# Performance work log

Hardware: AMD Instinct MI355X
Metric: run time of the kernel (lower is better)

Reference implementation:

```python
import jax, jax.numpy as jnp
import numpy as np
import math

V, D, H, L, T, B = 50257, 1024, 16, 8, 1024, 4
HD = D // H
EPS = 1e-5


def setup_inputs() -> dict:
    key = jax.random.key(0)
    ks = jax.random.split(key, 8)
    s = 0.02
    inp = {
        'context': jax.random.randint(ks[0], (B, T), 0, V, dtype=jnp.int32),
        'targets': jax.random.randint(ks[1], (B, T), 0, V, dtype=jnp.int32),
        'wte': jax.random.normal(ks[2], (V, D), jnp.float32) * s,  # tied with lm_head
        'wpe': jax.random.normal(ks[3], (T, D), jnp.float32) * s,
        'ln1_g': jnp.ones((L, D), jnp.float32), 'ln1_b': jnp.zeros((L, D), jnp.float32),
        'w_attn': jax.random.normal(ks[4], (L, 3 * D, D), jnp.float32) * s,
        'w_proj': jax.random.normal(ks[5], (L, D, D), jnp.float32) * s,
        'ln2_g': jnp.ones((L, D), jnp.float32), 'ln2_b': jnp.zeros((L, D), jnp.float32),
        'w_fc': jax.random.normal(ks[6], (L, 4 * D, D), jnp.float32) * s,
        'w_out': jax.random.normal(ks[7], (L, D, 4 * D), jnp.float32) * s,
        'lnf_g': jnp.ones((D,), jnp.float32), 'lnf_b': jnp.zeros((D,), jnp.float32),
    }
    return inp


def layer_norm(x, g, b):
    mu = jnp.mean(x, axis=-1, keepdims=True)
    var = jnp.var(x, axis=-1, keepdims=True)
    return (x - mu) * jax.lax.rsqrt(var + EPS) * g + b


def attention(x, w_attn, w_proj):
    # x: [B,T,D]; w_attn: [3D,D] (torch Linear convention: y = x @ W^T)
    qkv = x @ w_attn.T  # [B,T,3D]
    q, k, v = jnp.split(qkv, 3, axis=-1)
    q = q.reshape(B, T, H, HD).transpose(0, 2, 1, 3)  # [B,H,T,hd]
    k = k.reshape(B, T, H, HD).transpose(0, 2, 1, 3)
    v = v.reshape(B, T, H, HD).transpose(0, 2, 1, 3)
    att = jnp.einsum('bhtd,bhsd->bhts', q, k) * (1.0 / math.sqrt(HD))
    causal = jnp.tril(jnp.ones((T, T), dtype=bool))
    att = jnp.where(causal, att, -jnp.inf)
    att = jax.nn.softmax(att, axis=-1)
    y = jnp.einsum('bhts,bhsd->bhtd', att, v)
    y = y.transpose(0, 2, 1, 3).reshape(B, T, D)
    return y @ w_proj.T


def mlp(x, w_fc, w_out):
    h = jax.nn.gelu(x @ w_fc.T, approximate=False)  # exact GELU = torch nn.GELU()
    return h @ w_out.T


def reference(context, targets, wte, wpe, ln1_g, ln1_b, w_attn, w_proj,
              ln2_g, ln2_b, w_fc, w_out, lnf_g, lnf_b):
    x = wte[context] + wpe[jnp.arange(T)]  # [B,T,D]
    for i in range(L):
        x = x + attention(layer_norm(x, ln1_g[i], ln1_b[i]), w_attn[i], w_proj[i])
        x = x + mlp(layer_norm(x, ln2_g[i], ln2_b[i]), w_fc[i], w_out[i])
    x = layer_norm(x, lnf_g, lnf_b)
    logits = x @ wte.T  # tied lm_head, [B,T,V]
    # cross entropy with ignore_index=-1
    logp = jax.nn.log_softmax(logits, axis=-1)
    tgt = targets.reshape(-1)
    valid = tgt != -1
    safe_tgt = jnp.where(valid, tgt, 0)
    nll = -jnp.take_along_axis(logp.reshape(-1, V), safe_tgt[:, None], axis=-1)[:, 0]
    loss = jnp.sum(jnp.where(valid, nll, 0.0)) / jnp.maximum(jnp.sum(valid), 1)
    return logits, loss
```

## Files before the change

### kernel.cpp

```cpp
#include <hip/hip_runtime.h>
#include <cstdint>

#define V_SIZE 50257
#define V_PAD  50432
#define D_DIM  1024
#define H_NUM  16
#define L_NUM  8
#define T_LEN  1024
#define B_NUM  4
#define HD_DIM 64
#define M_ROWS 4096
#define LN_EPS 1e-5f

typedef __attribute__((ext_vector_type(8))) __bf16 bf16x8;
typedef __attribute__((ext_vector_type(4))) float f32x4;
typedef __attribute__((ext_vector_type(8))) unsigned short u16x8;

__device__ __forceinline__ unsigned short f2bf(float f) {
  unsigned u = __builtin_bit_cast(unsigned, f);
  u += 0x7fffu + ((u >> 16) & 1u);
  return (unsigned short)(u >> 16);
}

__device__ __forceinline__ void gload_lds16(const void* g, void* l) {
  typedef const __attribute__((address_space(1))) unsigned int* gp_t;
  typedef __attribute__((address_space(3))) unsigned int* lp_t;
  __builtin_amdgcn_global_load_lds((gp_t)g, (lp_t)l, 16, 0, 0);
}

#define BARSB() { __builtin_amdgcn_s_barrier(); __builtin_amdgcn_sched_barrier(0); }
#define LGKM0() { asm volatile("s_waitcnt lgkmcnt(0)" ::: "memory"); __builtin_amdgcn_sched_barrier(0); }

__global__ __launch_bounds__(256) void embed_kernel(const int* __restrict__ ctx,
                                                    const float* __restrict__ wte,
                                                    const float* __restrict__ wpe,
                                                    float* __restrict__ x) {
  int i = blockIdx.x * blockDim.x + threadIdx.x;
  if (i >= M_ROWS * D_DIM) return;
  int bt = i / D_DIM, d = i - bt * D_DIM;
  int t = bt & (T_LEN - 1);
  x[i] = wte[(size_t)ctx[bt] * D_DIM + d] + wpe[(size_t)t * D_DIM + d];
}

__global__ __launch_bounds__(256) void conv_layer_kernel(const float* __restrict__ wa,
                                                         const float* __restrict__ wp,
                                                         const float* __restrict__ wf,
                                                         const float* __restrict__ wo,
                                                         unsigned short* __restrict__ oa,
                                                         unsigned short* __restrict__ op,
                                                         unsigned short* __restrict__ of,
                                                         unsigned short* __restrict__ oo) {
  long i = (long)(blockIdx.x * 256 + threadIdx.x) * 8;
  const float* src; unsigned short* dst; long off;
  if (i < 3145728L)      { src = wa; dst = oa; off = i; }
  else if (i < 4194304L) { src = wp; dst = op; off = i - 3145728L; }
  else if (i < 8388608L) { src = wf; dst = of; off = i - 4194304L; }
  else                   { src = wo; dst = oo; off = i - 8388608L; }
  float4 v0 = *(const float4*)(src + off);
  float4 v1 = *(const float4*)(src + off + 4);
  u16x8 o;
  o[0] = f2bf(v0.x); o[1] = f2bf(v0.y); o[2] = f2bf(v0.z); o[3] = f2bf(v0.w);
  o[4] = f2bf(v1.x); o[5] = f2bf(v1.y); o[6] = f2bf(v1.z); o[7] = f2bf(v1.w);
  *(u16x8*)(dst + off) = o;
}

__global__ __launch_bounds__(256) void conv_kernel(const float* __restrict__ in,
                                                   unsigned short* __restrict__ out, long n) {
  long i = (long)(blockIdx.x * 256 + threadIdx.x) * 8;
  if (i >= n) return;
  float4 v0 = *(const float4*)(in + i);
  float4 v1 = *(const float4*)(in + i + 4);
  u16x8 o;
  o[0] = f2bf(v0.x); o[1] = f2bf(v0.y); o[2] = f2bf(v0.z); o[3] = f2bf(v0.w);
  o[4] = f2bf(v1.x); o[5] = f2bf(v1.y); o[6] = f2bf(v1.z); o[7] = f2bf(v1.w);
  *(u16x8*)(out + i) = o;
}

__global__ __launch_bounds__(256) void layernorm_kernel(const float* __restrict__ x,
                                                        const float* __restrict__ g,
                                                        const float* __restrict__ b,
                                                        unsigned short* __restrict__ o) {
  int r = blockIdx.x;
  int tid = threadIdx.x;
  const float* row = x + (size_t)r * D_DIM;
  float4 v = *(const float4*)(row + tid * 4);
  float s  = v.x + v.y + v.z + v.w;
  float s2 = v.x * v.x + v.y * v.y + v.z * v.z + v.w * v.w;
  #pragma unroll
  for (int off = 32; off; off >>= 1) {
    s  += __shfl_xor(s, off);
    s2 += __shfl_xor(s2, off);
  }
  __shared__ float a1[4], a2[4];
  int w = tid >> 6, lane = tid & 63;
  if (lane == 0) { a1[w] = s; a2[w] = s2; }
  __syncthreads();
  s  = a1[0] + a1[1] + a1[2] + a1[3];
  s2 = a2[0] + a2[1] + a2[2] + a2[3];
  float mu  = s * (1.0f / D_DIM);
  float var = s2 * (1.0f / D_DIM) - mu * mu;
  float rs  = rsqrtf(var + LN_EPS);
  int d = tid * 4;
  float4 gv = *(const float4*)(g + d);
  float4 bv = *(const float4*)(b + d);
  ushort4 ov;
  ov.x = f2bf((v.x - mu) * rs * gv.x + bv.x);
  ov.y = f2bf((v.y - mu) * rs * gv.y + bv.y);
  ov.z = f2bf((v.z - mu) * rs * gv.z + bv.z);
  ov.w = f2bf((v.w - mu) * rs * gv.w + bv.w);
  *(ushort4*)(o + (size_t)r * D_DIM + d) = ov;
}

template<int EPI>
__global__ __launch_bounds__(256) void mfma_gemm(const unsigned short* __restrict__ A,
                                                 const unsigned short* __restrict__ W,
                                                 const float* R, void* Cout,
                                                 int K, int ldc, int nreal) {
  __shared__ unsigned short As[128 * 32];
  __shared__ unsigned short Bs[128 * 32];
  const int tid  = threadIdx.x;
  const int wave = tid >> 6, lane = tid & 63;
  const int wr = wave >> 1, wc = wave & 1;
  const long row0 = (long)blockIdx.y * 128;
  const long col0 = (long)blockIdx.x * 128;
  f32x4 acc[4][4] = {};
  const int frow = lane & 15;
  const int fk   = (lane >> 4) * 8;
  const int b0 = wave * 2048 + lane * 16;
  for (int k0 = 0; k0 < K; k0 += 32) {
    #pragma unroll
    for (int c = 0; c < 2; ++c) {
      int b = b0 + c * 1024;
      int r = b >> 6, ke = (b & 63) >> 1;
      gload_lds16(A + (row0 + r) * (long)K + k0 + ke, (char*)As + b);
      gload_lds16(W + (col0 + r) * (long)K + k0 + ke, (char*)Bs + b);
    }
    __syncthreads();
    bf16x8 af[4], bfr[4];
    #pragma unroll
    for (int i = 0; i < 4; ++i)
      af[i] = *(const bf16x8*)(As + (wr * 64 + i * 16 + frow) * 32 + fk);
    #pragma unroll
    for (int j = 0; j < 4; ++j)
      bfr[j] = *(const bf16x8*)(Bs + (wc * 64 + j * 16 + frow) * 32 + fk);
    #pragma unroll
    for (int i = 0; i < 4; ++i)
      #pragma unroll
      for (int j = 0; j < 4; ++j)
        acc[i][j] = __builtin_amdgcn_mfma_f32_16x16x32_bf16(af[i], bfr[j], acc[i][j], 0, 0, 0);
    __syncthreads();
  }
  const int crow = (lane >> 4) * 4;
  const int ccol = lane & 15;
  #pragma unroll
  for (int i = 0; i < 4; ++i) {
    #pragma unroll
    for (int r = 0; r < 4; ++r) {
      long row = row0 + wr * 64 + i * 16 + crow + r;
      #pragma unroll
      for (int j = 0; j < 4; ++j) {
        long col = col0 + wc * 64 + j * 16 + ccol;
        float v = acc[i][j][r];
        if (EPI == 1) {
          ((float*)Cout)[row * (long)ldc + col] = v + R[row * (long)ldc + col];
        } else {
          ((float*)Cout)[row * (long)ldc + col] = v;
        }
      }
    }
  }
}

__device__ __forceinline__ void stage_chunk8(const unsigned short* __restrict__ base,
                                             long rbase, int K, long gk,
                                             char* cb, int tid) {
  #pragma unroll
  for (int j = 0; j < 2; ++j) {
    int db = j * 8192 + tid * 16;
    int lb = db ^ (((db >> 7) & 3) << 4);
    long r = lb >> 6;
    int e = (lb & 63) >> 1;
    gload_lds16(base + (rbase + r) * (long)K + gk + e, cb + db);
  }
}

__device__ __forceinline__ bf16x8 rdfrag(const char* cb, int rr, int lhi) {
  int p = (rr << 6) + (lhi << 4);
  p ^= ((rr >> 1) & 3) << 4;
  return *(const bf16x8*)(cb + p);
}

template<int EPI>
__global__ __launch_bounds__(512, 1) void gemm8p(const unsigned short* __restrict__ A,
                                                 const unsigned short* __restrict__ W,
                                                 void* Cout, int K, int ldc, int nreal,
                                                 int nbx, int xcd) {
  __shared__ char lds[131072];
  const int tid  = threadIdx.x;
  const int lane = tid & 63;
  const int wave = tid >> 6;
  const int wr = wave >> 2, wc = wave & 3;
  const int lhi = lane >> 4, llo = lane & 15;
  int bid = blockIdx.x;
  if (xcd) { int per = (int)gridDim.x >> 3; bid = (bid & 7) * per + (bid >> 3); }
  const int brow = bid % nbx;
  const int bcol = bid / nbx;
  const long row0 = (long)brow * 256;
  const long col0 = (long)bcol * 256;
  char* Ab0 = (char*)lds;
  char* Bb0 = (char*)lds + 65536;
  const int nt = K >> 6;

  stage_chunk8(A, row0, K, 0,  Ab0,         tid);
  stage_chunk8(W, col0, K, 0,  Bb0,         tid);
  stage_chunk8(A, row0, K, 32, Ab0 + 16384, tid);
  stage_chunk8(W, col0, K, 32, Bb0 + 16384, tid);
  if (nt > 1) {
    stage_chunk8(W, col0, K, 64, Bb0 + 32768, tid);
    stage_chunk8(A, row0, K, 64, Ab0 + 32768, tid);
    stage_chunk8(W, col0, K, 96, Bb0 + 49152, tid);
    asm volatile("s_waitcnt vmcnt(10)" ::: "memory");
  } else {
    asm volatile("s_waitcnt vmcnt(0)" ::: "memory");
  }
  BARSB();

  f32x4 acc[8][4] = {};
  bf16x8 bb[4];
  for (int t = 0; t < nt; ++t) {
    char* Ac = Ab0 + (t & 1) * 32768;
    char* Bc = Bb0 + (t & 1) * 32768;
    char* An = Ab0 + ((t + 1) & 1) * 32768;
    bf16x8 aa[4];
    #pragma unroll
    for (int m = 0; m < 4; ++m) aa[m] = rdfrag(Ac, wr * 128 + m * 16 + llo, lhi);
    #pragma unroll
    for (int n = 0; n < 4; ++n) bb[n] = rdfrag(Bc, wc * 64 + n * 16 + llo, lhi);
    if (t + 1 < nt) stage_chunk8(A, row0, K, (long)(t + 1) * 64 + 32, An + 16384, tid);
    BARSB(); LGKM0();
    __builtin_amdgcn_s_setprio(1);
    #pragma unroll
    for (int m = 0; m < 4; ++m)
      #pragma unroll
      for (int n = 0; n < 4; ++n)
        acc[m][n] = __builtin_amdgcn_mfma_f32_16x16x32_bf16(aa[m], bb[n], acc[m][n], 0, 0, 0);
    __builtin_amdgcn_s_setprio(0);
    BARSB();
    #pragma unroll
    for (int m = 0; m < 4; ++m) aa[m] = rdfrag(Ac, wr * 128 + 64 + m * 16 + llo, lhi);
    if (t + 2 < nt) stage_chunk8(W, col0, K, (long)(t + 2) * 64, Bc, tid);
    BARSB(); LGKM0();
    __builtin_amdgcn_s_setprio(1);
    #pragma unroll
    for (int m = 0; m < 4; ++m)
      #pragma unroll
      for (int n = 0; n < 4; ++n)
        acc[m + 4][n] = __builtin_amdgcn_mfma_f32_16x16x32_bf16(aa[m], bb[n], acc[m + 4][n], 0, 0, 0);
    __builtin_amdgcn_s_setprio(0);
    if (t <= nt - 3)      { asm volatile("s_waitcnt vmcnt(10)" ::: "memory"); }
    else if (t == nt - 2) { asm volatile("s_waitcnt vmcnt(8)"  ::: "memory"); }
    else                  { asm volatile("s_waitcnt vmcnt(0)"  ::: "memory"); }
    BARSB();
    #pragma unroll
    for (int m = 0; m < 4; ++m) aa[m] = rdfrag(Ac + 16384, wr * 128 + m * 16 + llo, lhi);
    #pragma unroll
    for (int n = 0; n < 4; ++n) bb[n] = rdfrag(Bc + 16384, wc * 64 + n * 16 + llo, lhi);
    if (t + 2 < nt) stage_chunk8(A, row0, K, (long)(t + 2) * 64, Ac, tid);
    BARSB(); LGKM0();
    __builtin_amdgcn_s_setprio(1);
    #pragma unroll
    for (int m = 0; m < 4; ++m)
      #pragma unroll
      for (int n = 0; n < 4; ++n)
        acc[m][n] = __builtin_amdgcn_mfma_f32_16x16x32_bf16(aa[m], bb[n], acc[m][n], 0, 0, 0);
    __builtin_amdgcn_s_setprio(0);
    BARSB();
    #pragma unroll
    for (int m = 0; m < 4; ++m) aa[m] = rdfrag(Ac + 16384, wr * 128 + 64 + m * 16 + llo, lhi);
    if (t + 2 < nt) stage_chunk8(W, col0, K, (long)(t + 2) * 64 + 32, Bc + 16384, tid);
    BARSB(); LGKM0();
    __builtin_amdgcn_s_setprio(1);
    #pragma unroll
    for (int m = 0; m < 4; ++m)
      #pragma unroll
      for (int n = 0; n < 4; ++n)
        acc[m + 4][n] = __builtin_amdgcn_mfma_f32_16x16x32_bf16(aa[m], bb[n], acc[m + 4][n], 0, 0, 0);
    __builtin_amdgcn_s_setprio(0);
    if (t <= nt - 3)      { asm volatile("s_waitcnt vmcnt(10)" ::: "memory"); }
    else if (t == nt - 2) { asm volatile("s_waitcnt vmcnt(4)"  ::: "memory"); }
    else                  { asm volatile("s_waitcnt vmcnt(0)"  ::: "memory"); }
    BARSB();
  }

  #pragma unroll
  for (int mi = 0; mi < 8; ++mi) {
    #pragma unroll
    for (int rg = 0; rg < 4; ++rg) {
      long row = row0 + wr * 128 + mi * 16 + lhi * 4 + rg;
      #pragma unroll
      for (int n = 0; n < 4; ++n) {
        long col = col0 + wc * 64 + n * 16 + llo;
        float v = acc[mi][n][rg];
        if (EPI == 0) {
          if (col < nreal) ((float*)Cout)[row * (long)ldc + col] = v;
        } else if (EPI == 2) {
          float gl = 0.5f * v * (1.0f + erff(v * 0.70710678118654752440f));
          ((unsigned short*)Cout)[row * (long)ldc + col] = f2bf(gl);
        } else {
          ((unsigned short*)Cout)[row * (long)ldc + col] = f2bf(v);
        }
      }
    }
  }
}

__global__ __launch_bounds__(256) void flash_attn_kernel(const unsigned short* __restrict__ qkv,
                                                         unsigned short* __restrict__ y) {
  __shared__ unsigned short Kls[64 * 64];
  __shared__ unsigned short Vtls[64 * 64];
  __shared__ unsigned short Pls[4][16 * 64];
  const int tid = threadIdx.x, wave = tid >> 6, lane = tid & 63;
  const int qt = blockIdx.x;
  const int h = blockIdx.y & (H_NUM - 1), b = blockIdx.y >> 4;
  const int q0 = qt * 64;
  const int lhi = lane >> 4, llo = lane & 15;

  const int qrow = q0 + wave * 16 + llo;
  const unsigned short* qptr =
      qkv + ((size_t)(b * T_LEN + qrow)) * 3072 + h * HD_DIM + lhi * 8;
  const bf16x8 qa0 = *(const bf16x8*)qptr;
  const bf16x8 qa1 = *(const bf16x8*)(qptr + 32);

  f32x4 o[4] = {};
  float m[4] = {-1e30f, -1e30f, -1e30f, -1e30f};
  float l[4] = {0.f, 0.f, 0.f, 0.f};

  const unsigned short* kg = qkv + (size_t)b * T_LEN * 3072 + D_DIM + h * HD_DIM;
  const unsigned short* vg = kg + D_DIM;

  const int krow = tid >> 2, kcol = (tid & 3) * 16;
  const int vs0 = (tid >> 3) * 2, vd0 = (tid & 7) * 8;

  const int ntiles = qt + 1;
  for (int st = 0; st < ntiles; ++st) {
    const int s0 = st * 64;
    {
      const unsigned short* src = kg + (size_t)(s0 + krow) * 3072 + kcol;
      u16x8 a = *(const u16x8*)src;
      u16x8 c = *(const u16x8*)(src + 8);
      int base = krow * 128 + kcol * 2;
      int sw = (krow & 7) << 4;
      *(u16x8*)((char*)Kls + ((base) ^ sw))      = a;
      *(u16x8*)((char*)Kls + ((base + 16) ^ sw)) = c;
    }
    {
      const unsigned short* src = vg + (size_t)(s0 + vs0) * 3072 + vd0;
      u16x8 a = *(const u16x8*)src;
      u16x8 c = *(const u16x8*)(src + 3072);
      #pragma unroll
      for (int j = 0; j < 8; ++j) {
        int d = vd0 + j;
        unsigned val = (unsigned)a[j] | ((unsigned)c[j] << 16);
        *(unsigned*)((char*)Vtls + ((d * 128 + vs0 * 2) ^ ((d & 7) << 4))) = val;
      }
    }
    __syncthreads();

    f32x4 s_acc[4] = {};
    #pragma unroll
    for (int kt = 0; kt < 4; ++kt) {
      int kr = kt * 16 + llo;
      int sw = (kr & 7) << 4;
      bf16x8 kb0 = *(const bf16x8*)((char*)Kls + ((kr * 128 + lhi * 16) ^ sw));
      bf16x8 kb1 = *(const bf16x8*)((char*)Kls + ((kr * 128 + 64 + lhi * 16) ^ sw));
      s_acc[kt] = __builtin_amdgcn_mfma_f32_16x16x32_bf16(qa0, kb0, s_acc[kt], 0, 0, 0);
      s_acc[kt] = __builtin_amdgcn_mfma_f32_16x16x32_bf16(qa1, kb1, s_acc[kt], 0, 0, 0);
    }

    float p[4][4];
    float tmax[4] = {-1e30f, -1e30f, -1e30f, -1e30f};
    const int qg = q0 + wave * 16 + lhi * 4;
    #pragma unroll
    for (int kt = 0; kt < 4; ++kt) {
      int ks = s0 + kt * 16 + llo;
      #pragma unroll
      for (int r = 0; r < 4; ++r) {
        float sv = (ks <= qg + r) ? s_acc[kt][r] * 0.125f : -1e30f;
        p[kt][r] = sv;
        tmax[r] = fmaxf(tmax[r], sv);
      }
    }
    #pragma unroll
    for (int r = 0; r < 4; ++r) {
      #pragma unroll
      for (int off = 1; off < 16; off <<= 1)
        tmax[r] = fmaxf(tmax[r], __shfl_xor(tmax[r], off));
      float mn = fmaxf(m[r], tmax[r]);
      float corr = __expf(m[r] - mn);
      m[r] = mn;
      float ps = 0.f;
      #pragma unroll
      for (int kt = 0; kt < 4; ++kt) {
        p[kt][r] = __expf(p[kt][r] - mn);
        ps += p[kt][r];
      }
      #pragma unroll
      for (int off = 1; off < 16; off <<= 1)
        ps += __shfl_xor(ps, off);
      l[r] = l[r] * corr + ps;
      #pragma unroll
      for (int dt = 0; dt < 4; ++dt) o[dt][r] *= corr;
    }

    unsigned short* pw = Pls[wave];
    #pragma unroll
    for (int r = 0; r < 4; ++r) {
      int q = lhi * 4 + r;
      int sw = (q & 7) << 4;
      #pragma unroll
      for (int kt = 0; kt < 4; ++kt) {
        int k = kt * 16 + llo;
        *(unsigned short*)((char*)pw + ((q * 128 + k * 2) ^ sw)) = f2bf(p[kt][r]);
      }
    }
    asm volatile("s_waitcnt lgkmcnt(0)" ::: "memory");

    int psw = (llo & 7) << 4;
    bf16x8 pa0 = *(const bf16x8*)((char*)pw + ((llo * 128 + lhi * 16) ^ psw));
    bf16x8 pa1 = *(const bf16x8*)((char*)pw + ((llo * 128 + 64 + lhi * 16) ^ psw));
    #pragma unroll
    for (int dt = 0; dt < 4; ++dt) {
      int vr = dt * 16 + llo;
      int sw = (vr & 7) << 4;
      bf16x8 vb0 = *(const bf16x8*)((char*)Vtls + ((vr * 128 + lhi * 16) ^ sw));
      bf16x8 vb1 = *(const bf16x8*)((char*)Vtls + ((vr * 128 + 64 + lhi * 16) ^ sw));
      o[dt] = __builtin_amdgcn_mfma_f32_16x16x32_bf16(pa0, vb0, o[dt], 0, 0, 0);
      o[dt] = __builtin_amdgcn_mfma_f32_16x16x32_bf16(pa1, vb1, o[dt], 0, 0, 0);
    }
    __syncthreads();
  }

  #pragma unroll
  for (int r = 0; r < 4; ++r) {
    long row = q0 + wave * 16 + lhi * 4 + r;
    float inv = 1.0f / l[r];
    #pragma unroll
    for (int dt = 0; dt < 4; ++dt) {
      long col = h * HD_DIM + dt * 16 + llo;
      y[(row + (size_t)b * T_LEN) * D_DIM + col] = f2bf(o[dt][r] * inv);
    }
  }
}

__global__ __launch_bounds__(256) void loss_rows_kernel(const float* __restrict__ logits,
                                                        const int* __restrict__ tgt,
                                                        float* __restrict__ nll,
                                                        float* __restrict__ vld) {
  int r = blockIdx.x;
  int tid = threadIdx.x;
  const float* row = logits + (size_t)r * V_SIZE;
  float lm = -1e30f, ls = 0.f;
  for (int i = tid; i < V_SIZE; i += 256) {
    float v = row[i];
    float nm = fmaxf(lm, v);
    ls = ls * __expf(lm - nm) + __expf(v - nm);
    lm = nm;
  }
  #pragma unroll
  for (int off = 1; off < 64; off <<= 1) {
    float om = __shfl_xor(lm, off);
    float os = __shfl_xor(ls, off);
    float nm = fmaxf(lm, om);
    ls = ls * __expf(lm - nm) + os * __expf(om - nm);
    lm = nm;
  }
  __shared__ float sm[4], ss[4];
  int w = tid >> 6, lane = tid & 63;
  if (lane == 0) { sm[w] = lm; ss[w] = ls; }
  __syncthreads();
  if (tid == 0) {
    lm = sm[0]; ls = ss[0];
    #pragma unroll
    for (int i = 1; i < 4; ++i) {
      float nm = fmaxf(lm, sm[i]);
      ls = ls * __expf(lm - nm) + ss[i] * __expf(sm[i] - nm);
      lm = nm;
    }
    int tg = tgt[r];
    if (tg != -1) { nll[r] = lm + logf(ls) - row[tg]; vld[r] = 1.0f; }
    else          { nll[r] = 0.f;                     vld[r] = 0.f; }
  }
}

__global__ __launch_bounds__(256) void loss_reduce_kernel(const float* __restrict__ nll,
                                                          const float* __restrict__ vld,
                                                          float* __restrict__ out) {
  int tid = threadIdx.x;
  float s = 0.f, c = 0.f;
  for (int i = tid; i < M_ROWS; i += 256) { s += nll[i]; c += vld[i]; }
  #pragma unroll
  for (int off = 32; off; off >>= 1) { s += __shfl_xor(s, off); c += __shfl_xor(c, off); }
  __shared__ float s1[4], s2[4];
  int w = tid >> 6, lane = tid & 63;
  if (lane == 0) { s1[w] = s; s2[w] = c; }
  __syncthreads();
  if (tid == 0) {
    s = s1[0] + s1[1] + s1[2] + s1[3];
    c = s2[0] + s2[1] + s2[2] + s2[3];
    out[0] = s / fmaxf(c, 1.0f);
  }
}

extern "C" void kernel_launch(void* const* d_in, const int* in_sizes, int n_in,
                              void* d_out, int out_size, void* d_ws, size_t ws_size,
                              hipStream_t stream) {
  const int*   ctx    = (const int*)d_in[0];
  const int*   tgt    = (const int*)d_in[1];
  const float* wte    = (const float*)d_in[2];
  const float* wpe    = (const float*)d_in[3];
  const float* ln1_g  = (const float*)d_in[4];
  const float* ln1_b  = (const float*)d_in[5];
  const float* w_attn = (const float*)d_in[6];
  const float* w_proj = (const float*)d_in[7];
  const float* ln2_g  = (const float*)d_in[8];
  const float* ln2_b  = (const float*)d_in[9];
  const float* w_fc   = (const float*)d_in[10];
  const float* w_out  = (const float*)d_in[11];
  const float* lnf_g  = (const float*)d_in[12];
  const float* lnf_b  = (const float*)d_in[13];

  float* outp   = (float*)d_out;
  float* logits = outp;
  float* loss   = outp + (size_t)M_ROWS * V_SIZE;

  char* ws = (char*)d_ws;
  float*          x      = (float*)(ws + 0);
  unsigned short* xn     = (unsigned short*)(ws + 16777216);
  unsigned short* qkv    = (unsigned short*)(ws + 25165824);
  unsigned short* y      = (unsigned short*)(ws + 50331648);
  unsigned short* h      = (unsigned short*)(ws + 58720256);
  unsigned short* wa_bf  = (unsigned short*)(ws + 92274688);
  unsigned short* wp_bf  = (unsigned short*)(ws + 98566144);
  unsigned short* wf_bf  = (unsigned short*)(ws + 100663296);
  unsigned short* wo_bf  = (unsigned short*)(ws + 109051904);
  unsigned short* wte_bf = (unsigned short*)(ws + 25165824);
  float*          nll    = (float*)(ws + 128450560);
  float*          vld    = (float*)(ws + 128466944);

  embed_kernel<<<(M_ROWS * D_DIM + 255) / 256, 256, 0, stream>>>(ctx, wte, wpe, x);

  for (int l = 0; l < L_NUM; ++l) {
    conv_layer_kernel<<<6144, 256, 0, stream>>>(
        w_attn + (size_t)l * 3 * D_DIM * D_DIM, w_proj + (size_t)l * D_DIM * D_DIM,
        w_fc + (size_t)l * 4 * D_DIM * D_DIM, w_out + (size_t)l * D_DIM * 4 * D_DIM,
        wa_bf, wp_bf, wf_bf, wo_bf);
    layernorm_kernel<<<M_ROWS, 256, 0, stream>>>(x, ln1_g + l * D_DIM, ln1_b + l * D_DIM, xn);
    gemm8p<3><<<12 * 16, 512, 0, stream>>>(
        xn, wa_bf, qkv, D_DIM, 3 * D_DIM, 3 * D_DIM, 16, 1);
    flash_attn_kernel<<<dim3(T_LEN / 64, B_NUM * H_NUM), 256, 0, stream>>>(qkv, y);
    mfma_gemm<1><<<dim3(D_DIM / 128, M_ROWS / 128), 256, 0, stream>>>(
        y, wp_bf, x, x, D_DIM, D_DIM, D_DIM);
    layernorm_kernel<<<M_ROWS, 256, 0, stream>>>(x, ln2_g + l * D_DIM, ln2_b + l * D_DIM, xn);
    gemm8p<2><<<16 * 16, 512, 0, stream>>>(
        xn, wf_bf, h, D_DIM, 4 * D_DIM, 4 * D_DIM, 16, 1);
    mfma_gemm<1><<<dim3(D_DIM / 128, M_ROWS / 128), 256, 0, stream>>>(
        h, wo_bf, x, x, 4 * D_DIM, D_DIM, D_DIM);
  }

  layernorm_kernel<<<M_ROWS, 256, 0, stream>>>(x, lnf_g, lnf_b, xn);
  conv_kernel<<<25129, 256, 0, stream>>>(wte, wte_bf, (long)V_SIZE * D_DIM);
  hipMemsetAsync(wte_bf + (size_t)V_SIZE * D_DIM, 0,
                 (size_t)(V_PAD - V_SIZE) * D_DIM * sizeof(unsigned short), stream);
  gemm8p<0><<<197 * 16, 512, 0, stream>>>(
      xn, wte_bf, logits, D_DIM, V_SIZE, V_SIZE, 16, 1);
  loss_rows_kernel<<<M_ROWS, 256, 0, stream>>>(logits, tgt, nll, vld);
  loss_reduce_kernel<<<1, 256, 0, stream>>>(nll, vld, loss);
}
```

Baseline: 3.490 ms.

## Software-pipeline LDS fragment reads against MFMAs in 256x256 GEMM main loop

```diff
diff --git a/kernel.cpp b/kernel.cpp
--- a/kernel.cpp
+++ b/kernel.cpp
@@ -28,8 +28,12 @@
   __builtin_amdgcn_global_load_lds((gp_t)g, (lp_t)l, 16, 0, 0);
 }
 
+__device__ __forceinline__ f32x4 mfma16(bf16x8 a, bf16x8 b, f32x4 c) {
+  return __builtin_amdgcn_mfma_f32_16x16x32_bf16(a, b, c, 0, 0, 0);
+}
+
 #define BARSB() { __builtin_amdgcn_s_barrier(); __builtin_amdgcn_sched_barrier(0); }
-#define LGKM0() { asm volatile("s_waitcnt lgkmcnt(0)" ::: "memory"); __builtin_amdgcn_sched_barrier(0); }
+#define SCHB()  __builtin_amdgcn_sched_barrier(0)
 
 __global__ __launch_bounds__(256) void embed_kernel(const int* __restrict__ ctx,
                                                     const float* __restrict__ wte,
@@ -147,7 +151,7 @@
     for (int i = 0; i < 4; ++i)
       #pragma unroll
       for (int j = 0; j < 4; ++j)
-        acc[i][j] = __builtin_amdgcn_mfma_f32_16x16x32_bf16(af[i], bfr[j], acc[i][j], 0, 0, 0);
+        acc[i][j] = mfma16(af[i], bfr[j], acc[i][j]);
     __syncthreads();
   }
   const int crow = (lane >> 4) * 4;
@@ -211,84 +215,99 @@
   char* Bb0 = (char*)lds + 65536;
   const int nt = K >> 6;
 
+  stage_chunk8(W, col0, K, 0,  Bb0,         tid);
   stage_chunk8(A, row0, K, 0,  Ab0,         tid);
-  stage_chunk8(W, col0, K, 0,  Bb0,         tid);
+  stage_chunk8(W, col0, K, 32, Bb0 + 16384, tid);
   stage_chunk8(A, row0, K, 32, Ab0 + 16384, tid);
-  stage_chunk8(W, col0, K, 32, Bb0 + 16384, tid);
-  if (nt > 1) {
-    stage_chunk8(W, col0, K, 64, Bb0 + 32768, tid);
-    stage_chunk8(A, row0, K, 64, Ab0 + 32768, tid);
-    stage_chunk8(W, col0, K, 96, Bb0 + 49152, tid);
-    asm volatile("s_waitcnt vmcnt(10)" ::: "memory");
-  } else {
-    asm volatile("s_waitcnt vmcnt(0)" ::: "memory");
-  }
+  stage_chunk8(W, col0, K, 64, Bb0 + 32768, tid);
+  stage_chunk8(A, row0, K, 64, Ab0 + 32768, tid);
+  stage_chunk8(W, col0, K, 96, Bb0 + 49152, tid);
+  asm volatile("s_waitcnt vmcnt(10)" ::: "memory");
   BARSB();
 
+  const int arow  = wr * 128 + llo;
+  const int brow_ = wc * 64 + llo;
+
+  bf16x8 aa0[4], aa1[4], bb0[4], bb1[4];
+  #pragma unroll
+  for (int m = 0; m < 4; ++m) aa0[m] = rdfrag(Ab0, arow + m * 16, lhi);
+  #pragma unroll
+  for (int n = 0; n < 4; ++n) bb0[n] = rdfrag(Bb0, brow_ + n * 16, lhi);
+
   f32x4 acc[8][4] = {};
-  bf16x8 bb[4];
   for (int t = 0; t < nt; ++t) {
     char* Ac = Ab0 + (t & 1) * 32768;
     char* Bc = Bb0 + (t & 1) * 32768;
     char* An = Ab0 + ((t + 1) & 1) * 32768;
-    bf16x8 aa[4];
-    #pragma unroll
-    for (int m = 0; m < 4; ++m) aa[m] = rdfrag(Ac, wr * 128 + m * 16 + llo, lhi);
-    #pragma unroll
-    for (int n = 0; n < 4; ++n) bb[n] = rdfrag(Bc, wc * 64 + n * 16 + llo, lhi);
+    char* Bn = Bb0 + ((t + 1) & 1) * 32768;
+    #pragma unroll
+    for (int m = 0; m < 4; ++m) aa1[m] = rdfrag(Ac, arow + 64 + m * 16, lhi);
+    asm volatile("s_waitcnt lgkmcnt(4)" ::: "memory");
+    SCHB();
     if (t + 1 < nt) stage_chunk8(A, row0, K, (long)(t + 1) * 64 + 32, An + 16384, tid);
-    BARSB(); LGKM0();
     __builtin_amdgcn_s_setprio(1);
     #pragma unroll
     for (int m = 0; m < 4; ++m)
       #pragma unroll
       for (int n = 0; n < 4; ++n)
-        acc[m][n] = __builtin_amdgcn_mfma_f32_16x16x32_bf16(aa[m], bb[n], acc[m][n], 0, 0, 0);
+        acc[m][n] = mfma16(aa0[m], bb0[n], acc[m][n]);
     __builtin_amdgcn_s_setprio(0);
+    SCHB();
+    if (t < nt - 1) { asm volatile("s_waitcnt vmcnt(8)" ::: "memory"); }
+    else            { asm volatile("s_waitcnt vmcnt(0)" ::: "memory"); }
     BARSB();
     #pragma unroll
-    for (int m = 0; m < 4; ++m) aa[m] = rdfrag(Ac, wr * 128 + 64 + m * 16 + llo, lhi);
+    for (int m = 0; m < 4; ++m) aa0[m] = rdfrag(Ac + 16384, arow + m * 16, lhi);
+    #pragma unroll
+    for (int n = 0; n < 4; ++n) bb1[n] = rdfrag(Bc + 16384, brow_ + n * 16, lhi);
+    asm volatile("s_waitcnt lgkmcnt(8)" ::: "memory");
+    SCHB();
     if (t + 2 < nt) stage_chunk8(W, col0, K, (long)(t + 2) * 64, Bc, tid);
-    BARSB(); LGKM0();
     __builtin_amdgcn_s_setprio(1);
     #pragma unroll
     for (int m = 0; m < 4; ++m)
       #pragma unroll
       for (int n = 0; n < 4; ++n)
-        acc[m + 4][n] = __builtin_amdgcn_mfma_f32_16x16x32_bf16(aa[m], bb[n], acc[m + 4][n], 0, 0, 0);
+        acc[m + 4][n] = mfma16(aa1[m], bb0[n], acc[m + 4][n]);
     __builtin_amdgcn_s_setprio(0);
-    if (t <= nt - 3)      { asm volatile("s_waitcnt vmcnt(10)" ::: "memory"); }
-    else if (t == nt - 2) { asm volatile("s_waitcnt vmcnt(8)"  ::: "memory"); }
-    else                  { asm volatile("s_waitcnt vmcnt(0)"  ::: "memory"); }
+    SCHB();
     BARSB();
     #pragma unroll
-    for (int m = 0; m < 4; ++m) aa[m] = rdfrag(Ac + 16384, wr * 128 + m * 16 + llo, lhi);
-    #pragma unroll
-    for (int n = 0; n < 4; ++n) bb[n] = rdfrag(Bc + 16384, wc * 64 + n * 16 + llo, lhi);
+    for (int m = 0; m < 4; ++m) aa1[m] = rdfrag(Ac + 16384, arow + 64 + m * 16, lhi);
+    asm volatile("s_waitcnt lgkmcnt(4)" ::: "memory");
+    SCHB();
     if (t + 2 < nt) stage_chunk8(A, row0, K, (long)(t + 2) * 64, Ac, tid);
-    BARSB(); LGKM0();
     __builtin_amdgcn_s_setprio(1);
     #pragma unroll
     for (int m = 0; m < 4; ++m)
       #pragma unroll
       for (int n = 0; n < 4; ++n)
-        acc[m][n] = __builtin_amdgcn_mfma_f32_16x16x32_bf16(aa[m], bb[n], acc[m][n], 0, 0, 0);
+        acc[m][n] = mfma16(aa0[m], bb1[n], acc[m][n]);
     __builtin_amdgcn_s_setprio(0);
+    SCHB();
+    if (t <= nt - 3)      { asm volatile("s_waitcnt vmcnt(8)" ::: "memory"); }
+    else if (t == nt - 2) { asm volatile("s_waitcnt vmcnt(4)" ::: "memory"); }
+    else                  { asm volatile("s_waitcnt vmcnt(0)" ::: "memory"); }
     BARSB();
-    #pragma unroll
-    for (int m = 0; m < 4; ++m) aa[m] = rdfrag(Ac + 16384, wr * 128 + 64 + m * 16 + llo, lhi);
+    if (t + 1 < nt) {
+      #pragma unroll
+      for (int m = 0; m < 4; ++m) aa0[m] = rdfrag(An, arow + m * 16, lhi);
+      #pragma unroll
+      for (int n = 0; n < 4; ++n) bb0[n] = rdfrag(Bn, brow_ + n * 16, lhi);
+      asm volatile("s_waitcnt lgkmcnt(8)" ::: "memory");
+    } else {
+      asm volatile("s_waitcnt lgkmcnt(0)" ::: "memory");
+    }
+    SCHB();
     if (t + 2 < nt) stage_chunk8(W, col0, K, (long)(t + 2) * 64 + 32, Bc + 16384, tid);
-    BARSB(); LGKM0();
     __builtin_amdgcn_s_setprio(1);
     #pragma unroll
     for (int m = 0; m < 4; ++m)
       #pragma unroll
       for (int n = 0; n < 4; ++n)
-        acc[m + 4][n] = __builtin_amdgcn_mfma_f32_16x16x32_bf16(aa[m], bb[n], acc[m + 4][n], 0, 0, 0);
+        acc[m + 4][n] = mfma16(aa1[m], bb1[n], acc[m + 4][n]);
     __builtin_amdgcn_s_setprio(0);
-    if (t <= nt - 3)      { asm volatile("s_waitcnt vmcnt(10)" ::: "memory"); }
-    else if (t == nt - 2) { asm volatile("s_waitcnt vmcnt(4)"  ::: "memory"); }
-    else                  { asm volatile("s_waitcnt vmcnt(0)"  ::: "memory"); }
+    SCHB();
     BARSB();
   }
 
@@ -373,8 +392,8 @@
       int sw = (kr & 7) << 4;
       bf16x8 kb0 = *(const bf16x8*)((char*)Kls + ((kr * 128 + lhi * 16) ^ sw));
       bf16x8 kb1 = *(const bf16x8*)((char*)Kls + ((kr * 128 + 64 + lhi * 16) ^ sw));
-      s_acc[kt] = __builtin_amdgcn_mfma_f32_16x16x32_bf16(qa0, kb0, s_acc[kt], 0, 0, 0);
-      s_acc[kt] = __builtin_amdgcn_mfma_f32_16x16x32_bf16(qa1, kb1, s_acc[kt], 0, 0, 0);
+      s_acc[kt] = mfma16(qa0, kb0, s_acc[kt]);
+      s_acc[kt] = mfma16(qa1, kb1, s_acc[kt]);
     }
 
     float p[4][4];
@@ -434,8 +453,8 @@
       int sw = (vr & 7) << 4;
       bf16x8 vb0 = *(const bf16x8*)((char*)Vtls + ((vr * 128 + lhi * 16) ^ sw));
       bf16x8 vb1 = *(const bf16x8*)((char*)Vtls + ((vr * 128 + 64 + lhi * 16) ^ sw));
-      o[dt] = __builtin_amdgcn_mfma_f32_16x16x32_bf16(pa0, vb0, o[dt], 0, 0, 0);
-      o[dt] = __builtin_amdgcn_mfma_f32_16x16x32_bf16(pa1, vb1, o[dt], 0, 0, 0);
+      o[dt] = mfma16(pa0, vb0, o[dt]);
+      o[dt] = mfma16(pa1, vb1, o[dt]);
     }
     __syncthreads();
   }
```

New measurement: 3.443 ms. Within noise of the previous version (-1.3%).
